# Optimization experiments

Hardware: AMD Instinct MI355X
Metric: run time of the kernel (lower is better)

Reference implementation:

```python
import jax, jax.numpy as jnp
import numpy as np

I_P = 8  # input_patch == output_patch


def extract_patches(x, i_p=I_P):
    # x: (B, N, C, H, W) -> (r, N*i_p*i_p, B, C), matching nn.Unfold(i_p, 1, 0, i_p)
    # followed by rearrange '(b n) (c i) r -> r (n i) b c' with i = h*w row-major.
    B, N, C, H, W = x.shape
    s1, s2 = H // i_p, W // i_p
    p = x.reshape(B, N, C, s1, i_p, s2, i_p)
    p = jnp.transpose(p, (3, 5, 1, 4, 6, 0, 2))  # (s1, s2, N, ph, pw, B, C)
    return p.reshape(s1 * s2, N * i_p * i_p, B, C)


def setup_inputs() -> dict:
    key = jax.random.key(0)
    ks = jax.random.split(key, 8)
    B, N, C, H = 1, 5, 3, 256
    inputs = jax.random.normal(ks[0], (B, N, C, H, H), jnp.float32)
    outputs = jax.random.normal(ks[1], (B, N, C, H, H), jnp.float32)
    # q/k projections of nn.MultiheadAttention(3, 1); v_proj and out_proj are frozen identity.
    Wq = jax.random.normal(ks[2], (3, 3), jnp.float32) * 0.5
    Wk = jax.random.normal(ks[3], (3, 3), jnp.float32) * 0.5
    bq = jax.random.normal(ks[4], (3,), jnp.float32) * 0.05
    bk = jax.random.normal(ks[5], (3,), jnp.float32) * 0.05
    bv = jnp.zeros((3,), jnp.float32)  # in_proj_bias for v initialised to zero
    return {
        "inputs": inputs,
        "outputs": outputs,
        "Wq": Wq,
        "Wk": Wk,
        "bq": bq,
        "bk": bk,
        "bv": bv,
        "loss_diff": jnp.float32(0.5),
        "step": 10,
        "max_steps": 100,
    }


def reference(inputs, outputs, Wq, Wk, bq, bk, bv, loss_diff, step, max_steps):
    B, N, C, H, W = inputs.shape
    i_p = I_P
    s = H // i_p
    mid = N // 2

    # (r, L, 3) with L = N*i_p^2; batch dim B==1 squeezed.
    X = extract_patches(inputs)[:, :, 0, :]
    Y = extract_patches(outputs)[:, :, 0, :]

    # The per-frame attention calls concatenated over frames equal a single
    # self-attention with Q=K=V=in_patches_flat (softmax is row-wise in queries).
    q = (X @ Wq.T + bq) / jnp.sqrt(jnp.float32(3.0))  # head_dim = 3
    k = X @ Wk.T + bk
    v = X + bv  # v_proj is identity (frozen)
    scores = jnp.einsum("rld,rmd->rlm", q, k)          # (r, L, L)
    attn = jax.nn.softmax(scores, axis=-1)
    out = jnp.einsum("rlm,rmd->rld", attn, v)           # out_proj identity, bias 0

    r = out.shape[0]
    # '(n h w) bs d -> (bs n) d h w' with bs=1  ->  (r, N, 3, i_p, i_p)
    align = out.reshape(r, N, i_p, i_p, 3).transpose(0, 1, 4, 2, 3)
    nin = Y.reshape(r, N, i_p, i_p, 3).transpose(0, 1, 4, 2, 3)

    per_patch_mse = lambda a, b: jnp.mean((a - b) ** 2, axis=(1, 2, 3, 4))
    mid_loss = jnp.sum(per_patch_mse(jnp.broadcast_to(nin[:, mid:mid + 1], align.shape), align))
    all_loss = jnp.sum(per_patch_mse(nin, align))
    coeff = loss_diff * (1.0 - step / max_steps) ** 10

    rec = jnp.mean(align, axis=1)  # (r, 3, i_p, i_p)
    rec_image = rec.reshape(s, s, 3, i_p, i_p).transpose(2, 0, 3, 1, 4).reshape(1, 3, H, W)
    rec_loss = jnp.mean((outputs[:, mid] - rec_image) ** 2)

    loss = mid_loss + coeff * all_loss + rec_loss
    return loss, rec_image
```

## Files before the change

### kernel.cpp

```cpp
#include <hip/hip_runtime.h>

#define HW    256
#define PLANE (256*256)
#define MID   2
#define NF    5
#define VTS   328

typedef float f32x4 __attribute__((ext_vector_type(4)));
typedef short s16x8 __attribute__((ext_vector_type(8)));

__device__ __forceinline__ float hw_exp2(float x) {
#if __has_builtin(__builtin_amdgcn_exp2f)
    return __builtin_amdgcn_exp2f(x);
#else
    float r; asm("v_exp_f32 %0, %1" : "=v"(r) : "v"(x)); return r;
#endif
}

__device__ __forceinline__ unsigned int f2bf(float f) {
    unsigned int u = __float_as_uint(f);
    u += 0x7FFF + ((u >> 16) & 1);
    return u >> 16;
}

__device__ __forceinline__ s16x8 mk_frag4(uint2 lo) {
    union { s16x8 v; unsigned int u[4]; } c;
    c.u[0] = lo.x; c.u[1] = lo.y; c.u[2] = 0; c.u[3] = 0;
    return c.v;
}
__device__ __forceinline__ s16x8 mk_frag8(unsigned int u0, unsigned int u1,
                                          unsigned int u2, unsigned int u3) {
    union { s16x8 v; unsigned int u[4]; } c;
    c.u[0] = u0; c.u[1] = u1; c.u[2] = u2; c.u[3] = u3;
    return c.v;
}

__global__ __launch_bounds__(256) void attn_mfma_kernel(
    const float* __restrict__ in,
    const float* __restrict__ outp,
    const float* __restrict__ Wq,
    const float* __restrict__ Wk,
    const float* __restrict__ bq,
    const float* __restrict__ bk,
    const float* __restrict__ bv,
    const float* __restrict__ loss_diff,
    const int*   __restrict__ step,
    const int*   __restrict__ max_steps,
    float* __restrict__ d_out)
{
    __shared__ __align__(16) unsigned short Kbf[320 * 4];
    __shared__ __align__(16) unsigned short Qbf[320 * 4];
    __shared__ __align__(16) unsigned short Vt[16 * VTS];
    __shared__ __align__(16) float oLDS[320 * 4];
    __shared__ float red[4];

    const int tid  = threadIdx.x;
    const int w    = tid >> 6;
    const int lane = tid & 63;
    const int col  = lane & 15;
    const int quad = lane >> 4;
    const int r    = blockIdx.x;
    const int s1   = r >> 5, s2 = r & 31;

    {
        unsigned int* v32 = (unsigned int*)Vt;
        for (int idx = 3 * (VTS / 2) + tid; idx < 16 * (VTS / 2); idx += 256)
            v32[idx] = (idx < 4 * (VTS / 2)) ? 0x3F803F80u : 0u;
    }

    const float QS = 0.57735026918962576f * 1.44269504088896340f;
    const float bv0 = bv[0], bv1 = bv[1], bv2 = bv[2];
    for (int t = tid; t < 320; t += 256) {
        const int n = t >> 6, i = t & 63;
        const int pix = (s1 * 8 + (i >> 3)) * HW + s2 * 8 + (i & 7);
        const float x0 = in[(n * 3 + 0) * PLANE + pix];
        const float x1 = in[(n * 3 + 1) * PLANE + pix];
        const float x2 = in[(n * 3 + 2) * PLANE + pix];
        const float k0 = x0 * Wk[0] + x1 * Wk[1] + x2 * Wk[2] + bk[0];
        const float k1 = x0 * Wk[3] + x1 * Wk[4] + x2 * Wk[5] + bk[1];
        const float k2 = x0 * Wk[6] + x1 * Wk[7] + x2 * Wk[8] + bk[2];
        const float q0 = (x0 * Wq[0] + x1 * Wq[1] + x2 * Wq[2] + bq[0]) * QS;
        const float q1 = (x0 * Wq[3] + x1 * Wq[4] + x2 * Wq[5] + bq[1]) * QS;
        const float q2 = (x0 * Wq[6] + x1 * Wq[7] + x2 * Wq[8] + bq[2]) * QS;
        *(uint2*)&Kbf[t * 4] = make_uint2(f2bf(k0) | (f2bf(k1) << 16), f2bf(k2));
        *(uint2*)&Qbf[t * 4] = make_uint2(f2bf(q0) | (f2bf(q1) << 16), f2bf(q2));
        Vt[0 * VTS + t] = (unsigned short)f2bf(x0 + bv0);
        Vt[1 * VTS + t] = (unsigned short)f2bf(x1 + bv1);
        Vt[2 * VTS + t] = (unsigned short)f2bf(x2 + bv2);
    }
    __syncthreads();

    s16x8 qf[5];
#pragma unroll
    for (int u = 0; u < 5; ++u) {
        uint2 qr = *(const uint2*)&Qbf[((w * 5 + u) * 16 + col) * 4];
        if (quad != 0) { qr.x = 0; qr.y = 0; }
        qf[u] = mk_frag4(qr);
    }

    f32x4 acc[5];
#pragma unroll
    for (int u = 0; u < 5; ++u) acc[u] = (f32x4){0.f, 0.f, 0.f, 0.f};
    const f32x4 zero4 = (f32x4){0.f, 0.f, 0.f, 0.f};

    for (int kb = 0; kb < 10; ++kb) {
        uint2 kr0 = *(const uint2*)&Kbf[(kb * 32 + col) * 4];
        uint2 kr1 = *(const uint2*)&Kbf[(kb * 32 + 16 + col) * 4];
        if (quad != 0) { kr0.x = 0; kr0.y = 0; kr1.x = 0; kr1.y = 0; }
        const s16x8 a0 = mk_frag4(kr0);
        const s16x8 a1 = mk_frag4(kr1);
        const unsigned short* vp = &Vt[col * VTS + kb * 32 + quad * 4];
        const uint2 vlo = *(const uint2*)vp;
        const uint2 vhi = *(const uint2*)(vp + 16);
        const s16x8 vf = mk_frag8(vlo.x, vlo.y, vhi.x, vhi.y);
#pragma unroll
        for (int u = 0; u < 5; ++u) {
            f32x4 c0 = __builtin_amdgcn_mfma_f32_16x16x32_bf16(a0, qf[u], zero4, 0, 0, 0);
            f32x4 c1 = __builtin_amdgcn_mfma_f32_16x16x32_bf16(a1, qf[u], zero4, 0, 0, 0);
            const unsigned int p0 = (__float_as_uint(hw_exp2(c0[0])) >> 16) |
                                    (__float_as_uint(hw_exp2(c0[1])) & 0xFFFF0000u);
            const unsigned int p1 = (__float_as_uint(hw_exp2(c0[2])) >> 16) |
                                    (__float_as_uint(hw_exp2(c0[3])) & 0xFFFF0000u);
            const unsigned int p2 = (__float_as_uint(hw_exp2(c1[0])) >> 16) |
                                    (__float_as_uint(hw_exp2(c1[1])) & 0xFFFF0000u);
            const unsigned int p3 = (__float_as_uint(hw_exp2(c1[2])) >> 16) |
                                    (__float_as_uint(hw_exp2(c1[3])) & 0xFFFF0000u);
            const s16x8 pf = mk_frag8(p0, p1, p2, p3);
            acc[u] = __builtin_amdgcn_mfma_f32_16x16x32_bf16(pf, vf, acc[u], 0, 0, 0);
        }
    }

    if (col < 4) {
#pragma unroll
        for (int u = 0; u < 5; ++u) {
            const int tbase = (w * 5 + u) * 16 + quad * 4;
#pragma unroll
            for (int rr = 0; rr < 4; ++rr)
                oLDS[(tbase + rr) * 4 + col] = acc[u][rr];
        }
    }
    __syncthreads();

    float tl = 0.0f;
    const float tt = 1.0f - (float)step[0] / (float)max_steps[0];
    const float t2 = tt * tt, t4 = t2 * t2, t8 = t4 * t4;
    const float coeff = loss_diff[0] * t8 * t2;

    for (int t = tid; t < 320; t += 256) {
        const int n = t >> 6, i = t & 63;
        const int pix = (s1 * 8 + (i >> 3)) * HW + s2 * 8 + (i & 7);
        const float4 oa = *(const float4*)&oLDS[t * 4];
        const float inv = 1.0f / oa.w;
        const float o0 = oa.x * inv, o1 = oa.y * inv, o2 = oa.z * inv;
        const float y0  = outp[(n * 3 + 0) * PLANE + pix];
        const float y1  = outp[(n * 3 + 1) * PLANE + pix];
        const float y2  = outp[(n * 3 + 2) * PLANE + pix];
        const float ym0 = outp[(MID * 3 + 0) * PLANE + pix];
        const float ym1 = outp[(MID * 3 + 1) * PLANE + pix];
        const float ym2 = outp[(MID * 3 + 2) * PLANE + pix];
        const float d0 = ym0 - o0, d1 = ym1 - o1, d2 = ym2 - o2;
        const float e0 = y0 - o0,  e1 = y1 - o1,  e2 = y2 - o2;
        tl += (d0*d0 + d1*d1 + d2*d2 + coeff * (e0*e0 + e1*e1 + e2*e2)) * (1.0f / 960.0f);
    }

    if (tid < 192) {
        const int c = tid >> 6, ii = tid & 63;
        const int pix2 = (s1 * 8 + (ii >> 3)) * HW + s2 * 8 + (ii & 7);
        float rec = 0.0f;
#pragma unroll
        for (int n = 0; n < NF; ++n) {
            const int t = n * 64 + ii;
            rec += oLDS[t * 4 + c] / oLDS[t * 4 + 3];
        }
        rec *= 0.2f;
        d_out[1 + c * PLANE + pix2] = rec;
        const float ym = outp[(MID * 3 + c) * PLANE + pix2];
        const float dr = ym - rec;
        tl += dr * dr * (1.0f / 196608.0f);
    }

#pragma unroll
    for (int off = 32; off; off >>= 1) tl += __shfl_down(tl, off);
    if (lane == 0) red[w] = tl;
    __syncthreads();
    if (tid == 0) atomicAdd(d_out, red[0] + red[1] + red[2] + red[3]);
}

extern "C" void kernel_launch(void* const* d_in, const int* in_sizes, int n_in,
                              void* d_out, int out_size, void* d_ws, size_t ws_size,
                              hipStream_t stream) {
    const float* in        = (const float*)d_in[0];
    const float* outp      = (const float*)d_in[1];
    const float* Wq        = (const float*)d_in[2];
    const float* Wk        = (const float*)d_in[3];
    const float* bq        = (const float*)d_in[4];
    const float* bk        = (const float*)d_in[5];
    const float* bv        = (const float*)d_in[6];
    const float* loss_diff = (const float*)d_in[7];
    const int*   step      = (const int*)d_in[8];
    const int*   max_steps = (const int*)d_in[9];
    float* out = (float*)d_out;

    hipMemsetAsync(out, 0, sizeof(float), stream);

    attn_mfma_kernel<<<1024, 256, 0, stream>>>(
        in, outp, Wq, Wk, bq, bk, bv, loss_diff, step, max_steps, out);
}
```

Measured before the change: 99.77 us.

## Split each patch's queries across two blocks of five waves

Each patch position is now handled by two blocks, each covering half of the 64 query pixels per frame, and each block has 320 threads (one wave per frame) instead of 256. This doubles the grid to 2048 blocks and cuts per-wave MFMA/exp work from five query tiles to two, to raise parallelism and occupancy on the many CUs. The bf16 packing of exp results is also replaced with a single byte-permute instruction. The cost is that both blocks redundantly load inputs and rebuild the full K/V tiles in LDS, and there are more atomics on the loss scalar.

```diff
diff --git a/kernel.cpp b/kernel.cpp
--- a/kernel.cpp
+++ b/kernel.cpp
@@ -23,6 +23,10 @@
     return u >> 16;
 }
 
+__device__ __forceinline__ unsigned int pack_bf(float a, float b) {
+    return __builtin_amdgcn_perm(__float_as_uint(b), __float_as_uint(a), 0x07060302u);
+}
+
 __device__ __forceinline__ s16x8 mk_frag4(uint2 lo) {
     union { s16x8 v; unsigned int u[4]; } c;
     c.u[0] = lo.x; c.u[1] = lo.y; c.u[2] = 0; c.u[3] = 0;
@@ -35,7 +39,7 @@
     return c.v;
 }
 
-__global__ __launch_bounds__(256) void attn_mfma_kernel(
+__global__ __launch_bounds__(320) void attn_mfma_kernel(
     const float* __restrict__ in,
     const float* __restrict__ outp,
     const float* __restrict__ Wq,
@@ -51,26 +55,29 @@
     __shared__ __align__(16) unsigned short Kbf[320 * 4];
     __shared__ __align__(16) unsigned short Qbf[320 * 4];
     __shared__ __align__(16) unsigned short Vt[16 * VTS];
-    __shared__ __align__(16) float oLDS[320 * 4];
-    __shared__ float red[4];
+    __shared__ __align__(16) float oLDS[160 * 4];
+    __shared__ float red[NF];
 
     const int tid  = threadIdx.x;
     const int w    = tid >> 6;
     const int lane = tid & 63;
     const int col  = lane & 15;
     const int quad = lane >> 4;
-    const int r    = blockIdx.x;
+    const int b    = blockIdx.x;
+    const int r    = b >> 1;
+    const int h    = b & 1;
     const int s1   = r >> 5, s2 = r & 31;
 
     {
         unsigned int* v32 = (unsigned int*)Vt;
-        for (int idx = 3 * (VTS / 2) + tid; idx < 16 * (VTS / 2); idx += 256)
+        for (int idx = 3 * (VTS / 2) + tid; idx < 16 * (VTS / 2); idx += 320)
             v32[idx] = (idx < 4 * (VTS / 2)) ? 0x3F803F80u : 0u;
     }
 
     const float QS = 0.57735026918962576f * 1.44269504088896340f;
     const float bv0 = bv[0], bv1 = bv[1], bv2 = bv[2];
-    for (int t = tid; t < 320; t += 256) {
+    {
+        const int t = tid;
         const int n = t >> 6, i = t & 63;
         const int pix = (s1 * 8 + (i >> 3)) * HW + s2 * 8 + (i & 7);
         const float x0 = in[(n * 3 + 0) * PLANE + pix];
@@ -90,17 +97,17 @@
     }
     __syncthreads();
 
-    s16x8 qf[5];
-#pragma unroll
-    for (int u = 0; u < 5; ++u) {
-        uint2 qr = *(const uint2*)&Qbf[((w * 5 + u) * 16 + col) * 4];
+    s16x8 qf[2];
+#pragma unroll
+    for (int u = 0; u < 2; ++u) {
+        uint2 qr = *(const uint2*)&Qbf[(w * 64 + 32 * h + 16 * u + col) * 4];
         if (quad != 0) { qr.x = 0; qr.y = 0; }
         qf[u] = mk_frag4(qr);
     }
 
-    f32x4 acc[5];
-#pragma unroll
-    for (int u = 0; u < 5; ++u) acc[u] = (f32x4){0.f, 0.f, 0.f, 0.f};
+    f32x4 acc[2];
+    acc[0] = (f32x4){0.f, 0.f, 0.f, 0.f};
+    acc[1] = (f32x4){0.f, 0.f, 0.f, 0.f};
     const f32x4 zero4 = (f32x4){0.f, 0.f, 0.f, 0.f};
 
     for (int kb = 0; kb < 10; ++kb) {
@@ -114,17 +121,13 @@
         const uint2 vhi = *(const uint2*)(vp + 16);
         const s16x8 vf = mk_frag8(vlo.x, vlo.y, vhi.x, vhi.y);
 #pragma unroll
-        for (int u = 0; u < 5; ++u) {
+        for (int u = 0; u < 2; ++u) {
             f32x4 c0 = __builtin_amdgcn_mfma_f32_16x16x32_bf16(a0, qf[u], zero4, 0, 0, 0);
             f32x4 c1 = __builtin_amdgcn_mfma_f32_16x16x32_bf16(a1, qf[u], zero4, 0, 0, 0);
-            const unsigned int p0 = (__float_as_uint(hw_exp2(c0[0])) >> 16) |
-                                    (__float_as_uint(hw_exp2(c0[1])) & 0xFFFF0000u);
-            const unsigned int p1 = (__float_as_uint(hw_exp2(c0[2])) >> 16) |
-                                    (__float_as_uint(hw_exp2(c0[3])) & 0xFFFF0000u);
-            const unsigned int p2 = (__float_as_uint(hw_exp2(c1[0])) >> 16) |
-                                    (__float_as_uint(hw_exp2(c1[1])) & 0xFFFF0000u);
-            const unsigned int p3 = (__float_as_uint(hw_exp2(c1[2])) >> 16) |
-                                    (__float_as_uint(hw_exp2(c1[3])) & 0xFFFF0000u);
+            const unsigned int p0 = pack_bf(hw_exp2(c0[0]), hw_exp2(c0[1]));
+            const unsigned int p1 = pack_bf(hw_exp2(c0[2]), hw_exp2(c0[3]));
+            const unsigned int p2 = pack_bf(hw_exp2(c1[0]), hw_exp2(c1[1]));
+            const unsigned int p3 = pack_bf(hw_exp2(c1[2]), hw_exp2(c1[3]));
             const s16x8 pf = mk_frag8(p0, p1, p2, p3);
             acc[u] = __builtin_amdgcn_mfma_f32_16x16x32_bf16(pf, vf, acc[u], 0, 0, 0);
         }
@@ -132,8 +135,8 @@
 
     if (col < 4) {
 #pragma unroll
-        for (int u = 0; u < 5; ++u) {
-            const int tbase = (w * 5 + u) * 16 + quad * 4;
+        for (int u = 0; u < 2; ++u) {
+            const int tbase = w * 32 + 16 * u + quad * 4;
 #pragma unroll
             for (int rr = 0; rr < 4; ++rr)
                 oLDS[(tbase + rr) * 4 + col] = acc[u][rr];
@@ -146,10 +149,11 @@
     const float t2 = tt * tt, t4 = t2 * t2, t8 = t4 * t4;
     const float coeff = loss_diff[0] * t8 * t2;
 
-    for (int t = tid; t < 320; t += 256) {
-        const int n = t >> 6, i = t & 63;
-        const int pix = (s1 * 8 + (i >> 3)) * HW + s2 * 8 + (i & 7);
-        const float4 oa = *(const float4*)&oLDS[t * 4];
+    if (tid < 160) {
+        const int n = tid >> 5;
+        const int ii = 32 * h + (tid & 31);
+        const int pix = (s1 * 8 + (ii >> 3)) * HW + s2 * 8 + (ii & 7);
+        const float4 oa = *(const float4*)&oLDS[tid * 4];
         const float inv = 1.0f / oa.w;
         const float o0 = oa.x * inv, o1 = oa.y * inv, o2 = oa.z * inv;
         const float y0  = outp[(n * 3 + 0) * PLANE + pix];
@@ -160,30 +164,32 @@
         const float ym2 = outp[(MID * 3 + 2) * PLANE + pix];
         const float d0 = ym0 - o0, d1 = ym1 - o1, d2 = ym2 - o2;
         const float e0 = y0 - o0,  e1 = y1 - o1,  e2 = y2 - o2;
-        tl += (d0*d0 + d1*d1 + d2*d2 + coeff * (e0*e0 + e1*e1 + e2*e2)) * (1.0f / 960.0f);
-    }
-
-    if (tid < 192) {
-        const int c = tid >> 6, ii = tid & 63;
-        const int pix2 = (s1 * 8 + (ii >> 3)) * HW + s2 * 8 + (ii & 7);
-        float rec = 0.0f;
-#pragma unroll
-        for (int n = 0; n < NF; ++n) {
-            const int t = n * 64 + ii;
-            rec += oLDS[t * 4 + c] / oLDS[t * 4 + 3];
+        tl = (d0*d0 + d1*d1 + d2*d2 + coeff * (e0*e0 + e1*e1 + e2*e2)) * (1.0f / 960.0f);
+    } else if (tid < 256) {
+        const int t96 = tid - 160;
+        if (t96 < 96) {
+            const int c = t96 >> 5;
+            const int ii = 32 * h + (t96 & 31);
+            const int pix2 = (s1 * 8 + (ii >> 3)) * HW + s2 * 8 + (ii & 7);
+            float rec = 0.0f;
+#pragma unroll
+            for (int n = 0; n < NF; ++n) {
+                const int t = n * 32 + (t96 & 31);
+                rec += oLDS[t * 4 + c] / oLDS[t * 4 + 3];
+            }
+            rec *= 0.2f;
+            d_out[1 + c * PLANE + pix2] = rec;
+            const float ym = outp[(MID * 3 + c) * PLANE + pix2];
+            const float dr = ym - rec;
+            tl = dr * dr * (1.0f / 196608.0f);
         }
-        rec *= 0.2f;
-        d_out[1 + c * PLANE + pix2] = rec;
-        const float ym = outp[(MID * 3 + c) * PLANE + pix2];
-        const float dr = ym - rec;
-        tl += dr * dr * (1.0f / 196608.0f);
     }
 
 #pragma unroll
     for (int off = 32; off; off >>= 1) tl += __shfl_down(tl, off);
     if (lane == 0) red[w] = tl;
     __syncthreads();
-    if (tid == 0) atomicAdd(d_out, red[0] + red[1] + red[2] + red[3]);
+    if (tid == 0) atomicAdd(d_out, red[0] + red[1] + red[2] + red[3] + red[4]);
 }
 
 extern "C" void kernel_launch(void* const* d_in, const int* in_sizes, int n_in,
@@ -203,6 +209,6 @@
 
     hipMemsetAsync(out, 0, sizeof(float), stream);
 
-    attn_mfma_kernel<<<1024, 256, 0, stream>>>(
+    attn_mfma_kernel<<<2048, 320, 0, stream>>>(
         in, outp, Wq, Wk, bq, bk, bv, loss_diff, step, max_steps, out);
 }
```

Result: slower. 112.1 us (+12.4%).
